# Performance work log

Measured on AMD Instinct MI355X. Metric: run time of the kernel, lower is better.

## Reference

```python
import jax, jax.numpy as jnp
import numpy as np

C = 256
NUM_HEADS = 8
NUM_GROUPS = 32
EPS = 1e-5


def setup_inputs() -> dict:
    key = jax.random.key(0)
    ks = jax.random.split(key, 7)
    B, H, W = 2, 64, 64
    x = jax.random.normal(ks[0], (B, C, H, W), dtype=jnp.float32)
    norm_gamma = jnp.ones((C,), dtype=jnp.float32)
    norm_beta = jnp.zeros((C,), dtype=jnp.float32)
    # 1x1 convs == per-pixel linear layers; store weights as (out_ch, in_ch)
    qkv_w = jax.random.normal(ks[1], (3 * C, C), dtype=jnp.float32) * (1.0 / np.sqrt(C))
    qkv_b = jnp.zeros((3 * C,), dtype=jnp.float32)
    proj_w = jax.random.normal(ks[2], (C, C), dtype=jnp.float32) * (1.0 / np.sqrt(C))
    proj_b = jnp.zeros((C,), dtype=jnp.float32)
    return {"x": x, "norm_gamma": norm_gamma, "norm_beta": norm_beta,
            "qkv_w": qkv_w, "qkv_b": qkv_b, "proj_w": proj_w, "proj_b": proj_b}


def _group_norm(x, gamma, beta):
    B, Cc, H, W = x.shape
    xg = x.reshape(B, NUM_GROUPS, Cc // NUM_GROUPS, H, W)
    mean = xg.mean(axis=(2, 3, 4), keepdims=True)
    var = xg.var(axis=(2, 3, 4), keepdims=True)
    xn = ((xg - mean) * jax.lax.rsqrt(var + EPS)).reshape(B, Cc, H, W)
    return xn * gamma[None, :, None, None] + beta[None, :, None, None]


def reference(x, norm_gamma, norm_beta, qkv_w, qkv_b, proj_w, proj_b):
    B, Cc, H, W = x.shape
    hd = Cc // NUM_HEADS
    N = H * W

    h = _group_norm(x, norm_gamma, norm_beta)
    # 1x1 conv: (3C,C) x (B,C,H,W) -> (B,3C,H,W)
    qkv = jnp.einsum('oc,bchw->bohw', qkv_w, h) + qkv_b[None, :, None, None]
    q, k, v = jnp.split(qkv, 3, axis=1)

    def heads(t):  # (B,C,H,W) -> (B,heads,N,hd)
        return t.reshape(B, NUM_HEADS, hd, N).transpose(0, 1, 3, 2)

    q, k, v = heads(q), heads(k), heads(v)
    scale = hd ** (-0.5)
    attn = jax.nn.softmax(jnp.einsum('bhnd,bhmd->bhnm', q, k) * scale, axis=-1)
    out = jnp.einsum('bhnm,bhmd->bhnd', attn, v)  # (B,heads,N,hd)
    out = out.transpose(0, 1, 3, 2).reshape(B, Cc, H, W)
    out = jnp.einsum('oc,bchw->bohw', proj_w, out) + proj_b[None, :, None, None]
    return x + out
```

## Files before the change

kernel.cpp:

```cpp
#include <hip/hip_runtime.h>
#include <math.h>

#define C_    256
#define NH    8
#define HD_   32
#define NG    32
#define CPG   8
#define NPIX  4096
#define BATCH 2
#define EPSV  1e-5f
#define SLOG2 0.25503489f
#define MF    16.0f
#define KVB   128
#define KSTR  40
#define VSTR  136
#define KPS2  2048

typedef __bf16 bf16x8 __attribute__((ext_vector_type(8)));
typedef __bf16 bf16x4 __attribute__((ext_vector_type(4)));
typedef float  f32x4  __attribute__((ext_vector_type(4)));

__global__ __launch_bounds__(256) void prep_kernel(const float* __restrict__ x,
                                                   float* __restrict__ partial,
                                                   const float* __restrict__ qw,
                                                   const float* __restrict__ pw,
                                                   __bf16* __restrict__ wbq,
                                                   __bf16* __restrict__ wbp) {
    if (blockIdx.x >= 512) {
        const int i = ((blockIdx.x - 512) * 256 + threadIdx.x) * 4;
        const float* src;
        __bf16* dst;
        int off;
        if (i < 768 * 256) { src = qw; dst = wbq; off = i; }
        else { src = pw; dst = wbp; off = i - 768 * 256; }
        const float4 v = *(const float4*)(src + off);
        bf16x4 o;
        o[0] = (__bf16)v.x; o[1] = (__bf16)v.y; o[2] = (__bf16)v.z; o[3] = (__bf16)v.w;
        *(bf16x4*)(dst + off) = o;
        return;
    }
    const int bg = blockIdx.x >> 3;
    const int part = blockIdx.x & 7;
    const int b = bg >> 5, g = bg & 31;
    const float* __restrict__ xp = x + ((size_t)(b * C_ + g * CPG)) * NPIX;

    float s = 0.f, ss = 0.f;
    #pragma unroll
    for (int p = 0; p < 4; ++p) {
        const int i = part * 4096 + p * 1024 + threadIdx.x * 4;
        const float4 v = *(const float4*)(xp + i);
        s  += v.x + v.y + v.z + v.w;
        ss += v.x * v.x + v.y * v.y + v.z * v.z + v.w * v.w;
    }
    #pragma unroll
    for (int off = 32; off; off >>= 1) {
        s  += __shfl_down(s, off);
        ss += __shfl_down(ss, off);
    }
    __shared__ float ls[4], lss[4];
    const int wid = threadIdx.x >> 6, lane = threadIdx.x & 63;
    if (lane == 0) { ls[wid] = s; lss[wid] = ss; }
    __syncthreads();
    if (threadIdx.x == 0) {
        float S = 0.f, SS = 0.f;
        #pragma unroll
        for (int w = 0; w < 4; ++w) { S += ls[w]; SS += lss[w]; }
        partial[bg * 16 + part * 2 + 0] = S;
        partial[bg * 16 + part * 2 + 1] = SS;
    }
}

__global__ __launch_bounds__(256) void qkv_gemm_kernel(const __bf16* __restrict__ wbq,
                                                       const float* __restrict__ bias,
                                                       const float* __restrict__ x,
                                                       const float* __restrict__ partial,
                                                       const float* __restrict__ gamma,
                                                       const float* __restrict__ beta,
                                                       __bf16* __restrict__ Qb,
                                                       __bf16* __restrict__ Kb,
                                                       __bf16* __restrict__ Vb) {
    const int b = blockIdx.z;
    const int n0 = blockIdx.x * 64;
    __shared__ __align__(16) __bf16 tile[64][264];
    __shared__ float gstat[NG][2];

    if (threadIdx.x < NG) {
        float S = 0.f, SS = 0.f;
        #pragma unroll
        for (int p = 0; p < 8; ++p) {
            S  += partial[(b * NG + threadIdx.x) * 16 + p * 2 + 0];
            SS += partial[(b * NG + threadIdx.x) * 16 + p * 2 + 1];
        }
        const float inv_n = 1.0f / (float)(CPG * NPIX);
        const float mean = S * inv_n;
        const float var  = SS * inv_n - mean * mean;
        gstat[threadIdx.x][0] = mean;
        gstat[threadIdx.x][1] = rsqrtf(var + EPSV);
    }
    __syncthreads();

    {
        const int nn = (threadIdx.x & 15) * 4;
        #pragma unroll
        for (int p = 0; p < 16; ++p) {
            const int c = (threadIdx.x >> 4) + p * 16;
            const float4 v = *(const float4*)(x + ((size_t)(b * C_ + c)) * NPIX + n0 + nn);
            const int g = c >> 3;
            const float ga = gamma[c] * gstat[g][1];
            const float be = beta[c] - gstat[g][0] * ga;
            tile[nn + 0][c] = (__bf16)(v.x * ga + be);
            tile[nn + 1][c] = (__bf16)(v.y * ga + be);
            tile[nn + 2][c] = (__bf16)(v.z * ga + be);
            tile[nn + 3][c] = (__bf16)(v.w * ga + be);
        }
    }
    __syncthreads();

    const int wave = threadIdx.x >> 6, lane = threadIdx.x & 63;
    const int col = lane & 15, g = lane >> 4;
    const int m0 = blockIdx.y * 128 + wave * 32;

    f32x4 acc[2][4];
    #pragma unroll
    for (int i = 0; i < 2; ++i)
        #pragma unroll
        for (int j = 0; j < 4; ++j) acc[i][j] = (f32x4){0.f, 0.f, 0.f, 0.f};

    #pragma unroll
    for (int c0 = 0; c0 < C_; c0 += 32) {
        bf16x8 la[2], lb[4];
        #pragma unroll
        for (int mb = 0; mb < 2; ++mb)
            la[mb] = *(const bf16x8*)(wbq + (size_t)(m0 + mb * 16 + col) * C_ + c0 + g * 8);
        #pragma unroll
        for (int nb = 0; nb < 4; ++nb)
            lb[nb] = *(const bf16x8*)(&tile[nb * 16 + col][c0 + g * 8]);
        #pragma unroll
        for (int mb = 0; mb < 2; ++mb)
            #pragma unroll
            for (int nb = 0; nb < 4; ++nb)
                acc[mb][nb] = __builtin_amdgcn_mfma_f32_16x16x32_bf16(la[mb], lb[nb], acc[mb][nb], 0, 0, 0);
    }

    #pragma unroll
    for (int mb = 0; mb < 2; ++mb) {
        const int mbase = m0 + mb * 16 + 4 * g;
        const float4 b4 = *(const float4*)(bias + mbase);
        const int route = mbase >> 8;
        const int bh = b * NH + ((mbase >> 5) & 7);
        const int d0 = mbase & 31;
        #pragma unroll
        for (int nb = 0; nb < 4; ++nb) {
            const int n = n0 + nb * 16 + col;
            f32x4 v = acc[mb][nb];
            v[0] += b4.x; v[1] += b4.y; v[2] += b4.z; v[3] += b4.w;
            if (route == 0) {
                bf16x4 o;
                #pragma unroll
                for (int r = 0; r < 4; ++r) o[r] = (__bf16)(v[r] * SLOG2);
                *(bf16x4*)(Qb + (((size_t)bh * NPIX + n) << 5) + d0) = o;
            } else if (route == 1) {
                bf16x4 o;
                #pragma unroll
                for (int r = 0; r < 4; ++r) o[r] = (__bf16)v[r];
                *(bf16x4*)(Kb + (((size_t)bh * NPIX + n) << 5) + d0) = o;
            } else {
                #pragma unroll
                for (int r = 0; r < 4; ++r)
                    Vb[((size_t)bh * HD_ + d0 + r) * NPIX + n] = (__bf16)v[r];
            }
        }
    }
}

__global__ __launch_bounds__(512) void attn_kernel(const __bf16* __restrict__ Qb,
                                                   const __bf16* __restrict__ Kb,
                                                   const __bf16* __restrict__ Vb,
                                                   __bf16* __restrict__ aot) {
    __shared__ __align__(16) char smem[75776];
    __bf16 (*Ks)[2][KVB][KSTR] = (__bf16 (*)[2][KVB][KSTR])(smem);
    __bf16 (*Vs)[2][HD_][VSTR] = (__bf16 (*)[2][HD_][VSTR])(smem + 40960);
    float* pbuf = (float*)smem;

    const int id = blockIdx.x;
    const int h = id & 7;
    const int rest = id >> 3;
    const int b = rest >> 5;
    const int qt = rest & 31;

    const int wave = threadIdx.x >> 6, lane = threadIdx.x & 63;
    const int hw = wave >> 2, wv = wave & 3;
    const int col = lane & 15, g = lane >> 4;
    const int bh = b * NH + h;
    const int q0 = qt * 128 + wv * 32;

    const __bf16* __restrict__ qp = Qb + ((size_t)bh * NPIX + q0) * HD_;
    const __bf16* __restrict__ kp = Kb + ((size_t)bh * NPIX + hw * KPS2) * HD_;
    const __bf16* __restrict__ vp = Vb + (size_t)bh * HD_ * NPIX + hw * KPS2;

    const int sk_key = wv * 16 + (lane >> 2);
    const int sk_seg = (lane & 3) * 8;
    const int sv_d   = wv * 8 + (lane >> 3);
    const int sv_seg = (lane & 7) * 8;
    const int vslot  = (sv_seg & 32) + ((((sv_seg & 15) >> 2) << 3)) + (((sv_seg >> 4) & 1) << 2);
    const __bf16* __restrict__ kg = kp + (size_t)sk_key * HD_ + sk_seg;
    const __bf16* __restrict__ vg = vp + (size_t)sv_d * NPIX + sv_seg;

    const bf16x8 fq0 = *(const bf16x8*)(qp + col * HD_ + g * 8);
    const bf16x8 fq1 = *(const bf16x8*)(qp + (16 + col) * HD_ + g * 8);

    bf16x8 ones;
    #pragma unroll
    for (int j = 0; j < 8; ++j) ones[j] = (__bf16)1.0f;
    const f32x4 mfc = {-MF, -MF, -MF, -MF};

    f32x4 acc00 = {0.f,0.f,0.f,0.f}, acc01 = {0.f,0.f,0.f,0.f};
    f32x4 acc10 = {0.f,0.f,0.f,0.f}, acc11 = {0.f,0.f,0.f,0.f};
    f32x4 accL0 = {0.f,0.f,0.f,0.f}, accL1 = {0.f,0.f,0.f,0.f};

    {
        const bf16x8 rk0 = *(const bf16x8*)(kg);
        const bf16x8 rk1 = *(const bf16x8*)(kg + (size_t)64 * HD_);
        const bf16x8 rv0 = *(const bf16x8*)(vg);
        const bf16x8 rv1 = *(const bf16x8*)(vg + 64);
        *(bf16x8*)&Ks[hw][0][sk_key][sk_seg]      = rk0;
        *(bf16x8*)&Ks[hw][0][sk_key + 64][sk_seg] = rk1;
        bf16x4 lo, hi;
        #pragma unroll
        for (int j = 0; j < 4; ++j) { lo[j] = rv0[j]; hi[j] = rv0[4 + j]; }
        *(bf16x4*)&Vs[hw][0][sv_d][vslot]     = lo;
        *(bf16x4*)&Vs[hw][0][sv_d][vslot + 8] = hi;
        #pragma unroll
        for (int j = 0; j < 4; ++j) { lo[j] = rv1[j]; hi[j] = rv1[4 + j]; }
        *(bf16x4*)&Vs[hw][0][sv_d][vslot + 64]     = lo;
        *(bf16x4*)&Vs[hw][0][sv_d][vslot + 64 + 8] = hi;
    }
    __syncthreads();

    const int nt = KPS2 / KVB;
    for (int t = 0; t < nt; ++t) {
        const int cur = t & 1;
        bf16x8 nk0, nk1, nv0, nv1;
        const bool more = (t + 1 < nt);
        {
            const size_t koff = (size_t)(more ? (t + 1) * KVB : 0);
            nk0 = *(const bf16x8*)(kg + koff * HD_);
            nk1 = *(const bf16x8*)(kg + (koff + 64) * HD_);
            nv0 = *(const bf16x8*)(vg + koff);
            nv1 = *(const bf16x8*)(vg + koff + 64);
        }

        #pragma unroll
        for (int kk = 0; kk < KVB; kk += 32) {
            const bf16x8 fk0 = *(const bf16x8*)(&Ks[hw][cur][kk + col][g * 8]);
            const bf16x8 fk1 = *(const bf16x8*)(&Ks[hw][cur][kk + 16 + col][g * 8]);
            const bf16x8 fv0 = *(const bf16x8*)(&Vs[hw][cur][col][kk + 8 * g]);
            const bf16x8 fv1 = *(const bf16x8*)(&Vs[hw][cur][col + 16][kk + 8 * g]);

            f32x4 s00 = __builtin_amdgcn_mfma_f32_16x16x32_bf16(fk0, fq0, mfc, 0, 0, 0);
            f32x4 s10 = __builtin_amdgcn_mfma_f32_16x16x32_bf16(fk1, fq0, mfc, 0, 0, 0);
            f32x4 s01 = __builtin_amdgcn_mfma_f32_16x16x32_bf16(fk0, fq1, mfc, 0, 0, 0);
            f32x4 s11 = __builtin_amdgcn_mfma_f32_16x16x32_bf16(fk1, fq1, mfc, 0, 0, 0);

            float p0[8], p1[8];
            #pragma unroll
            for (int r = 0; r < 4; ++r) {
                p0[r]     = __builtin_amdgcn_exp2f(s00[r]);
                p0[4 + r] = __builtin_amdgcn_exp2f(s10[r]);
                p1[r]     = __builtin_amdgcn_exp2f(s01[r]);
                p1[4 + r] = __builtin_amdgcn_exp2f(s11[r]);
            }

            bf16x8 fp0, fp1;
            #pragma unroll
            for (int j = 0; j < 8; ++j) { fp0[j] = (__bf16)p0[j]; fp1[j] = (__bf16)p1[j]; }

            accL0 = __builtin_amdgcn_mfma_f32_16x16x32_bf16(ones, fp0, accL0, 0, 0, 0);
            accL1 = __builtin_amdgcn_mfma_f32_16x16x32_bf16(ones, fp1, accL1, 0, 0, 0);
            acc00 = __builtin_amdgcn_mfma_f32_16x16x32_bf16(fv0, fp0, acc00, 0, 0, 0);
            acc01 = __builtin_amdgcn_mfma_f32_16x16x32_bf16(fv1, fp0, acc01, 0, 0, 0);
            acc10 = __builtin_amdgcn_mfma_f32_16x16x32_bf16(fv0, fp1, acc10, 0, 0, 0);
            acc11 = __builtin_amdgcn_mfma_f32_16x16x32_bf16(fv1, fp1, acc11, 0, 0, 0);
        }

        if (more) {
            *(bf16x8*)&Ks[hw][cur ^ 1][sk_key][sk_seg]      = nk0;
            *(bf16x8*)&Ks[hw][cur ^ 1][sk_key + 64][sk_seg] = nk1;
            bf16x4 lo, hi;
            #pragma unroll
            for (int j = 0; j < 4; ++j) { lo[j] = nv0[j]; hi[j] = nv0[4 + j]; }
            *(bf16x4*)&Vs[hw][cur ^ 1][sv_d][vslot]     = lo;
            *(bf16x4*)&Vs[hw][cur ^ 1][sv_d][vslot + 8] = hi;
            #pragma unroll
            for (int j = 0; j < 4; ++j) { lo[j] = nv1[j]; hi[j] = nv1[4 + j]; }
            *(bf16x4*)&Vs[hw][cur ^ 1][sv_d][vslot + 64]     = lo;
            *(bf16x4*)&Vs[hw][cur ^ 1][sv_d][vslot + 64 + 8] = hi;
        }
        __syncthreads();
    }

    float l0 = accL0[0], l1 = accL1[0];

    if (hw == 1) {
        float* pp = pbuf + ((size_t)wv * 64 + lane) * 20;
        *(f32x4*)(pp + 0)  = acc00;
        *(f32x4*)(pp + 4)  = acc01;
        *(f32x4*)(pp + 8)  = acc10;
        *(f32x4*)(pp + 12) = acc11;
        pp[16] = l0; pp[17] = l1;
    }
    __syncthreads();
    if (hw == 0) {
        const float* pp = pbuf + ((size_t)wv * 64 + lane) * 20;
        const f32x4 b00 = *(const f32x4*)(pp + 0);
        const f32x4 b01 = *(const f32x4*)(pp + 4);
        const f32x4 b10 = *(const f32x4*)(pp + 8);
        const f32x4 b11 = *(const f32x4*)(pp + 12);
        #pragma unroll
        for (int r = 0; r < 4; ++r) {
            acc00[r] += b00[r]; acc01[r] += b01[r];
            acc10[r] += b10[r]; acc11[r] += b11[r];
        }
        const float inv0 = 1.0f / (l0 + pp[16]);
        const float inv1 = 1.0f / (l1 + pp[17]);
        const int cb = h * HD_ + 4 * g;
        {
            __bf16* op = aot + ((size_t)(b * NPIX) + q0 + col) * C_ + cb;
            bf16x4 o0, o1;
            #pragma unroll
            for (int r = 0; r < 4; ++r) { o0[r] = (__bf16)(acc00[r] * inv0); o1[r] = (__bf16)(acc01[r] * inv0); }
            *(bf16x4*)(op) = o0;
            *(bf16x4*)(op + 16) = o1;
        }
        {
            __bf16* op = aot + ((size_t)(b * NPIX) + q0 + 16 + col) * C_ + cb;
            bf16x4 o0, o1;
            #pragma unroll
            for (int r = 0; r < 4; ++r) { o0[r] = (__bf16)(acc10[r] * inv1); o1[r] = (__bf16)(acc11[r] * inv1); }
            *(bf16x4*)(op) = o0;
            *(bf16x4*)(op + 16) = o1;
        }
    }
}

__global__ __launch_bounds__(256) void proj_gemm_kernel(const __bf16* __restrict__ wbp,
                                                        const float* __restrict__ bias,
                                                        const __bf16* __restrict__ aot,
                                                        const float* __restrict__ x,
                                                        float* __restrict__ out) {
    const int b = blockIdx.z;
    const int wave = threadIdx.x >> 6, lane = threadIdx.x & 63;
    const int col = lane & 15, g = lane >> 4;
    const int n0 = blockIdx.x * 64 + (wave & 1) * 32;
    const int m0 = blockIdx.y * 64 + (wave >> 1) * 32;
    const __bf16* __restrict__ ap = aot + (size_t)b * NPIX * C_;

    f32x4 acc[2][2];
    #pragma unroll
    for (int i = 0; i < 2; ++i)
        #pragma unroll
        for (int j = 0; j < 2; ++j) acc[i][j] = (f32x4){0.f, 0.f, 0.f, 0.f};

    #pragma unroll
    for (int c0 = 0; c0 < C_; c0 += 32) {
        bf16x8 la[2], lb[2];
        #pragma unroll
        for (int mb = 0; mb < 2; ++mb)
            la[mb] = *(const bf16x8*)(wbp + (size_t)(m0 + mb * 16 + col) * C_ + c0 + g * 8);
        #pragma unroll
        for (int nb = 0; nb < 2; ++nb)
            lb[nb] = *(const bf16x8*)(ap + (size_t)(n0 + nb * 16 + col) * C_ + c0 + g * 8);
        #pragma unroll
        for (int mb = 0; mb < 2; ++mb)
            #pragma unroll
            for (int nb = 0; nb < 2; ++nb)
                acc[mb][nb] = __builtin_amdgcn_mfma_f32_16x16x32_bf16(la[mb], lb[nb], acc[mb][nb], 0, 0, 0);
    }

    #pragma unroll
    for (int mb = 0; mb < 2; ++mb) {
        const int mbase = m0 + mb * 16 + 4 * g;
        const float4 b4 = *(const float4*)(bias + mbase);
        const float bias_r[4] = {b4.x, b4.y, b4.z, b4.w};
        #pragma unroll
        for (int nb = 0; nb < 2; ++nb) {
            const int n = n0 + nb * 16 + col;
            #pragma unroll
            for (int r = 0; r < 4; ++r) {
                const size_t idx = ((size_t)(b * C_ + mbase + r)) * NPIX + n;
                out[idx] = acc[mb][nb][r] + bias_r[r] + x[idx];
            }
        }
    }
}

extern "C" void kernel_launch(void* const* d_in, const int* in_sizes, int n_in,
                              void* d_out, int out_size, void* d_ws, size_t ws_size,
                              hipStream_t stream) {
    (void)in_sizes; (void)n_in; (void)out_size; (void)ws_size;
    const float* x      = (const float*)d_in[0];
    const float* gamma  = (const float*)d_in[1];
    const float* beta   = (const float*)d_in[2];
    const float* qkv_w  = (const float*)d_in[3];
    const float* qkv_b  = (const float*)d_in[4];
    const float* proj_w = (const float*)d_in[5];
    const float* proj_b = (const float*)d_in[6];
    float* out = (float*)d_out;

    char* ws = (char*)d_ws;
    __bf16* wbq     = (__bf16*)(ws);
    __bf16* wbp     = (__bf16*)(ws + 0x60000);
    float*  partial = (float*) (ws + 0x80000);
    __bf16* Qb      = (__bf16*)(ws + 0x500000);
    __bf16* Kb      = (__bf16*)(ws + 0x900000);
    __bf16* Vb      = (__bf16*)(ws + 0xD00000);
    __bf16* aot     = (__bf16*)(ws + 0x1100000);

    prep_kernel<<<dim3(768), dim3(256), 0, stream>>>(x, partial, qkv_w, proj_w, wbq, wbp);
    qkv_gemm_kernel<<<dim3(NPIX / 64, 768 / 128, BATCH), dim3(256), 0, stream>>>(
        wbq, qkv_b, x, partial, gamma, beta, Qb, Kb, Vb);
    attn_kernel<<<dim3(32 * NH * BATCH), dim3(512), 0, stream>>>(Qb, Kb, Vb, aot);
    proj_gemm_kernel<<<dim3(NPIX / 64, C_ / 64, BATCH), dim3(256), 0, stream>>>(wbp, proj_b, aot, x, out);
}
```

Baseline: 79.10 us.

## Split attention keys four ways with 64 queries per wave

Reorganises the attention block so its 8 waves form four key-split groups of two, instead of two groups of four. Each wave now handles 64 queries instead of 32, with a smaller 64-key tile per step. Every K/V fragment read from shared memory is reused across twice as many queries, cutting LDS traffic per MFMA. The cost is more accumulator registers per wave, a larger shared-memory footprint, and a three-way partial-sum reduction at the end instead of one.

New measurement: 86.67 us. +9.6%, slower.

```diff
diff --git a/kernel.cpp b/kernel.cpp
--- a/kernel.cpp
+++ b/kernel.cpp
@@ -11,10 +11,10 @@
 #define EPSV  1e-5f
 #define SLOG2 0.25503489f
 #define MF    16.0f
-#define KVB   128
+#define KVB   64
 #define KSTR  40
-#define VSTR  136
-#define KPS2  2048
+#define VSTR  72
+#define KPS4  1024
 
 typedef __bf16 bf16x8 __attribute__((ext_vector_type(8)));
 typedef __bf16 bf16x4 __attribute__((ext_vector_type(4)));
@@ -177,7 +177,7 @@
                                                    const __bf16* __restrict__ Kb,
                                                    const __bf16* __restrict__ Vb,
                                                    __bf16* __restrict__ aot) {
-    __shared__ __align__(16) char smem[75776];
+    __shared__ __align__(16) char smem[77824];
     __bf16 (*Ks)[2][KVB][KSTR] = (__bf16 (*)[2][KVB][KSTR])(smem);
     __bf16 (*Vs)[2][HD_][VSTR] = (__bf16 (*)[2][HD_][VSTR])(smem + 40960);
     float* pbuf = (float*)smem;
@@ -189,42 +189,47 @@
     const int qt = rest & 31;
 
     const int wave = threadIdx.x >> 6, lane = threadIdx.x & 63;
-    const int hw = wave >> 2, wv = wave & 3;
+    const int hw = wave >> 1, wv = wave & 1;
     const int col = lane & 15, g = lane >> 4;
     const int bh = b * NH + h;
-    const int q0 = qt * 128 + wv * 32;
+    const int q0 = qt * 128 + wv * 64;
 
     const __bf16* __restrict__ qp = Qb + ((size_t)bh * NPIX + q0) * HD_;
-    const __bf16* __restrict__ kp = Kb + ((size_t)bh * NPIX + hw * KPS2) * HD_;
-    const __bf16* __restrict__ vp = Vb + (size_t)bh * HD_ * NPIX + hw * KPS2;
+    const __bf16* __restrict__ kp = Kb + ((size_t)bh * NPIX + hw * KPS4) * HD_;
+    const __bf16* __restrict__ vp = Vb + (size_t)bh * HD_ * NPIX + hw * KPS4;
 
     const int sk_key = wv * 16 + (lane >> 2);
     const int sk_seg = (lane & 3) * 8;
-    const int sv_d   = wv * 8 + (lane >> 3);
-    const int sv_seg = (lane & 7) * 8;
-    const int vslot  = (sv_seg & 32) + ((((sv_seg & 15) >> 2) << 3)) + (((sv_seg >> 4) & 1) << 2);
+    const int sv_d   = wv * 16 + (lane >> 2);
+    const int sv_seg = (lane & 3) * 8;
+    const int vslot  = (((sv_seg & 15) >> 2) << 3) + (((sv_seg >> 4) & 1) << 2);
     const __bf16* __restrict__ kg = kp + (size_t)sk_key * HD_ + sk_seg;
     const __bf16* __restrict__ vg = vp + (size_t)sv_d * NPIX + sv_seg;
 
-    const bf16x8 fq0 = *(const bf16x8*)(qp + col * HD_ + g * 8);
-    const bf16x8 fq1 = *(const bf16x8*)(qp + (16 + col) * HD_ + g * 8);
+    const bf16x8 fqA = *(const bf16x8*)(qp + col * HD_ + g * 8);
+    const bf16x8 fqB = *(const bf16x8*)(qp + (16 + col) * HD_ + g * 8);
+    const bf16x8 fqC = *(const bf16x8*)(qp + (32 + col) * HD_ + g * 8);
+    const bf16x8 fqD = *(const bf16x8*)(qp + (48 + col) * HD_ + g * 8);
 
     bf16x8 ones;
     #pragma unroll
     for (int j = 0; j < 8; ++j) ones[j] = (__bf16)1.0f;
     const f32x4 mfc = {-MF, -MF, -MF, -MF};
 
-    f32x4 acc00 = {0.f,0.f,0.f,0.f}, acc01 = {0.f,0.f,0.f,0.f};
-    f32x4 acc10 = {0.f,0.f,0.f,0.f}, acc11 = {0.f,0.f,0.f,0.f};
-    f32x4 accL0 = {0.f,0.f,0.f,0.f}, accL1 = {0.f,0.f,0.f,0.f};
+    f32x4 accA0 = {0.f,0.f,0.f,0.f}, accA1 = {0.f,0.f,0.f,0.f};
+    f32x4 accB0 = {0.f,0.f,0.f,0.f}, accB1 = {0.f,0.f,0.f,0.f};
+    f32x4 accC0 = {0.f,0.f,0.f,0.f}, accC1 = {0.f,0.f,0.f,0.f};
+    f32x4 accD0 = {0.f,0.f,0.f,0.f}, accD1 = {0.f,0.f,0.f,0.f};
+    f32x4 accLA = {0.f,0.f,0.f,0.f}, accLB = {0.f,0.f,0.f,0.f};
+    f32x4 accLC = {0.f,0.f,0.f,0.f}, accLD = {0.f,0.f,0.f,0.f};
 
     {
         const bf16x8 rk0 = *(const bf16x8*)(kg);
-        const bf16x8 rk1 = *(const bf16x8*)(kg + (size_t)64 * HD_);
+        const bf16x8 rk1 = *(const bf16x8*)(kg + (size_t)32 * HD_);
         const bf16x8 rv0 = *(const bf16x8*)(vg);
-        const bf16x8 rv1 = *(const bf16x8*)(vg + 64);
+        const bf16x8 rv1 = *(const bf16x8*)(vg + 32);
         *(bf16x8*)&Ks[hw][0][sk_key][sk_seg]      = rk0;
-        *(bf16x8*)&Ks[hw][0][sk_key + 64][sk_seg] = rk1;
+        *(bf16x8*)&Ks[hw][0][sk_key + 32][sk_seg] = rk1;
         bf16x4 lo, hi;
         #pragma unroll
         for (int j = 0; j < 4; ++j) { lo[j] = rv0[j]; hi[j] = rv0[4 + j]; }
@@ -232,12 +237,12 @@
         *(bf16x4*)&Vs[hw][0][sv_d][vslot + 8] = hi;
         #pragma unroll
         for (int j = 0; j < 4; ++j) { lo[j] = rv1[j]; hi[j] = rv1[4 + j]; }
-        *(bf16x4*)&Vs[hw][0][sv_d][vslot + 64]     = lo;
-        *(bf16x4*)&Vs[hw][0][sv_d][vslot + 64 + 8] = hi;
+        *(bf16x4*)&Vs[hw][0][sv_d][vslot + 32]     = lo;
+        *(bf16x4*)&Vs[hw][0][sv_d][vslot + 32 + 8] = hi;
     }
     __syncthreads();
 
-    const int nt = KPS2 / KVB;
+    const int nt = KPS4 / KVB;
     for (int t = 0; t < nt; ++t) {
         const int cur = t & 1;
         bf16x8 nk0, nk1, nv0, nv1;
@@ -245,9 +250,9 @@
         {
             const size_t koff = (size_t)(more ? (t + 1) * KVB : 0);
             nk0 = *(const bf16x8*)(kg + koff * HD_);
-            nk1 = *(const bf16x8*)(kg + (koff + 64) * HD_);
+            nk1 = *(const bf16x8*)(kg + (koff + 32) * HD_);
             nv0 = *(const bf16x8*)(vg + koff);
-            nv1 = *(const bf16x8*)(vg + koff + 64);
+            nv1 = *(const bf16x8*)(vg + koff + 32);
         }
 
         #pragma unroll
@@ -257,35 +262,45 @@
             const bf16x8 fv0 = *(const bf16x8*)(&Vs[hw][cur][col][kk + 8 * g]);
             const bf16x8 fv1 = *(const bf16x8*)(&Vs[hw][cur][col + 16][kk + 8 * g]);
 
-            f32x4 s00 = __builtin_amdgcn_mfma_f32_16x16x32_bf16(fk0, fq0, mfc, 0, 0, 0);
-            f32x4 s10 = __builtin_amdgcn_mfma_f32_16x16x32_bf16(fk1, fq0, mfc, 0, 0, 0);
-            f32x4 s01 = __builtin_amdgcn_mfma_f32_16x16x32_bf16(fk0, fq1, mfc, 0, 0, 0);
-            f32x4 s11 = __builtin_amdgcn_mfma_f32_16x16x32_bf16(fk1, fq1, mfc, 0, 0, 0);
-
-            float p0[8], p1[8];
+            f32x4 sA0 = __builtin_amdgcn_mfma_f32_16x16x32_bf16(fk0, fqA, mfc, 0, 0, 0);
+            f32x4 sA1 = __builtin_amdgcn_mfma_f32_16x16x32_bf16(fk1, fqA, mfc, 0, 0, 0);
+            f32x4 sB0 = __builtin_amdgcn_mfma_f32_16x16x32_bf16(fk0, fqB, mfc, 0, 0, 0);
+            f32x4 sB1 = __builtin_amdgcn_mfma_f32_16x16x32_bf16(fk1, fqB, mfc, 0, 0, 0);
+            f32x4 sC0 = __builtin_amdgcn_mfma_f32_16x16x32_bf16(fk0, fqC, mfc, 0, 0, 0);
+            f32x4 sC1 = __builtin_amdgcn_mfma_f32_16x16x32_bf16(fk1, fqC, mfc, 0, 0, 0);
+            f32x4 sD0 = __builtin_amdgcn_mfma_f32_16x16x32_bf16(fk0, fqD, mfc, 0, 0, 0);
+            f32x4 sD1 = __builtin_amdgcn_mfma_f32_16x16x32_bf16(fk1, fqD, mfc, 0, 0, 0);
+
+            bf16x8 fpA, fpB, fpC, fpD;
             #pragma unroll
             for (int r = 0; r < 4; ++r) {
-                p0[r]     = __builtin_amdgcn_exp2f(s00[r]);
-                p0[4 + r] = __builtin_amdgcn_exp2f(s10[r]);
-                p1[r]     = __builtin_amdgcn_exp2f(s01[r]);
-                p1[4 + r] = __builtin_amdgcn_exp2f(s11[r]);
+                fpA[r]     = (__bf16)__builtin_amdgcn_exp2f(sA0[r]);
+                fpA[4 + r] = (__bf16)__builtin_amdgcn_exp2f(sA1[r]);
+                fpB[r]     = (__bf16)__builtin_amdgcn_exp2f(sB0[r]);
+                fpB[4 + r] = (__bf16)__builtin_amdgcn_exp2f(sB1[r]);
+                fpC[r]     = (__bf16)__builtin_amdgcn_exp2f(sC0[r]);
+                fpC[4 + r] = (__bf16)__builtin_amdgcn_exp2f(sC1[r]);
+                fpD[r]     = (__bf16)__builtin_amdgcn_exp2f(sD0[r]);
+                fpD[4 + r] = (__bf16)__builtin_amdgcn_exp2f(sD1[r]);
             }
 
-            bf16x8 fp0, fp1;
-            #pragma unroll
-            for (int j = 0; j < 8; ++j) { fp0[j] = (__bf16)p0[j]; fp1[j] = (__bf16)p1[j]; }
-
-            accL0 = __builtin_amdgcn_mfma_f32_16x16x32_bf16(ones, fp0, accL0, 0, 0, 0);
-            accL1 = __builtin_amdgcn_mfma_f32_16x16x32_bf16(ones, fp1, accL1, 0, 0, 0);
-            acc00 = __builtin_amdgcn_mfma_f32_16x16x32_bf16(fv0, fp0, acc00, 0, 0, 0);
-            acc01 = __builtin_amdgcn_mfma_f32_16x16x32_bf16(fv1, fp0, acc01, 0, 0, 0);
-            acc10 = __builtin_amdgcn_mfma_f32_16x16x32_bf16(fv0, fp1, acc10, 0, 0, 0);
-            acc11 = __builtin_amdgcn_mfma_f32_16x16x32_bf16(fv1, fp1, acc11, 0, 0, 0);
+            accLA = __builtin_amdgcn_mfma_f32_16x16x32_bf16(ones, fpA, accLA, 0, 0, 0);
+            accLB = __builtin_amdgcn_mfma_f32_16x16x32_bf16(ones, fpB, accLB, 0, 0, 0);
+            accLC = __builtin_amdgcn_mfma_f32_16x16x32_bf16(ones, fpC, accLC, 0, 0, 0);
+            accLD = __builtin_amdgcn_mfma_f32_16x16x32_bf16(ones, fpD, accLD, 0, 0, 0);
+            accA0 = __builtin_amdgcn_mfma_f32_16x16x32_bf16(fv0, fpA, accA0, 0, 0, 0);
+            accA1 = __builtin_amdgcn_mfma_f32_16x16x32_bf16(fv1, fpA, accA1, 0, 0, 0);
+            accB0 = __builtin_amdgcn_mfma_f32_16x16x32_bf16(fv0, fpB, accB0, 0, 0, 0);
+            accB1 = __builtin_amdgcn_mfma_f32_16x16x32_bf16(fv1, fpB, accB1, 0, 0, 0);
+            accC0 = __builtin_amdgcn_mfma_f32_16x16x32_bf16(fv0, fpC, accC0, 0, 0, 0);
+            accC1 = __builtin_amdgcn_mfma_f32_16x16x32_bf16(fv1, fpC, accC1, 0, 0, 0);
+            accD0 = __builtin_amdgcn_mfma_f32_16x16x32_bf16(fv0, fpD, accD0, 0, 0, 0);
+            accD1 = __builtin_amdgcn_mfma_f32_16x16x32_bf16(fv1, fpD, accD1, 0, 0, 0);
         }
 
         if (more) {
             *(bf16x8*)&Ks[hw][cur ^ 1][sk_key][sk_seg]      = nk0;
-            *(bf16x8*)&Ks[hw][cur ^ 1][sk_key + 64][sk_seg] = nk1;
+            *(bf16x8*)&Ks[hw][cur ^ 1][sk_key + 32][sk_seg] = nk1;
             bf16x4 lo, hi;
             #pragma unroll
             for (int j = 0; j < 4; ++j) { lo[j] = nv0[j]; hi[j] = nv0[4 + j]; }
@@ -293,50 +308,50 @@
             *(bf16x4*)&Vs[hw][cur ^ 1][sv_d][vslot + 8] = hi;
             #pragma unroll
             for (int j = 0; j < 4; ++j) { lo[j] = nv1[j]; hi[j] = nv1[4 + j]; }
-            *(bf16x4*)&Vs[hw][cur ^ 1][sv_d][vslot + 64]     = lo;
-            *(bf16x4*)&Vs[hw][cur ^ 1][sv_d][vslot + 64 + 8] = hi;
+            *(bf16x4*)&Vs[hw][cur ^ 1][sv_d][vslot + 32]     = lo;
+            *(bf16x4*)&Vs[hw][cur ^ 1][sv_d][vslot + 32 + 8] = hi;
         }
         __syncthreads();
     }
 
-    float l0 = accL0[0], l1 = accL1[0];
-
-    if (hw == 1) {
-        float* pp = pbuf + ((size_t)wv * 64 + lane) * 20;
-        *(f32x4*)(pp + 0)  = acc00;
-        *(f32x4*)(pp + 4)  = acc01;
-        *(f32x4*)(pp + 8)  = acc10;
-        *(f32x4*)(pp + 12) = acc11;
-        pp[16] = l0; pp[17] = l1;
+    if (hw != 0) {
+        float* pp = pbuf + ((size_t)((hw - 1) * 128 + wv * 64 + lane)) * 36;
+        *(f32x4*)(pp + 0)  = accA0; *(f32x4*)(pp + 4)  = accA1;
+        *(f32x4*)(pp + 8)  = accB0; *(f32x4*)(pp + 12) = accB1;
+        *(f32x4*)(pp + 16) = accC0; *(f32x4*)(pp + 20) = accC1;
+        *(f32x4*)(pp + 24) = accD0; *(f32x4*)(pp + 28) = accD1;
+        pp[32] = accLA[0]; pp[33] = accLB[0]; pp[34] = accLC[0]; pp[35] = accLD[0];
     }
     __syncthreads();
     if (hw == 0) {
-        const float* pp = pbuf + ((size_t)wv * 64 + lane) * 20;
-        const f32x4 b00 = *(const f32x4*)(pp + 0);
-        const f32x4 b01 = *(const f32x4*)(pp + 4);
-        const f32x4 b10 = *(const f32x4*)(pp + 8);
-        const f32x4 b11 = *(const f32x4*)(pp + 12);
-        #pragma unroll
-        for (int r = 0; r < 4; ++r) {
-            acc00[r] += b00[r]; acc01[r] += b01[r];
-            acc10[r] += b10[r]; acc11[r] += b11[r];
-        }
-        const float inv0 = 1.0f / (l0 + pp[16]);
-        const float inv1 = 1.0f / (l1 + pp[17]);
+        float lA = accLA[0], lB = accLB[0], lC = accLC[0], lD = accLD[0];
+        #pragma unroll
+        for (int s = 0; s < 3; ++s) {
+            const float* pp = pbuf + ((size_t)(s * 128 + wv * 64 + lane)) * 36;
+            const f32x4 a0 = *(const f32x4*)(pp + 0),  a1 = *(const f32x4*)(pp + 4);
+            const f32x4 b0 = *(const f32x4*)(pp + 8),  b1 = *(const f32x4*)(pp + 12);
+            const f32x4 c0 = *(const f32x4*)(pp + 16), c1 = *(const f32x4*)(pp + 20);
+            const f32x4 d0 = *(const f32x4*)(pp + 24), d1 = *(const f32x4*)(pp + 28);
+            #pragma unroll
+            for (int r = 0; r < 4; ++r) {
+                accA0[r] += a0[r]; accA1[r] += a1[r];
+                accB0[r] += b0[r]; accB1[r] += b1[r];
+                accC0[r] += c0[r]; accC1[r] += c1[r];
+                accD0[r] += d0[r]; accD1[r] += d1[r];
+            }
+            lA += pp[32]; lB += pp[33]; lC += pp[34]; lD += pp[35];
+        }
+        const float iA = 1.0f / lA, iB = 1.0f / lB, iC = 1.0f / lC, iD = 1.0f / lD;
         const int cb = h * HD_ + 4 * g;
-        {
-            __bf16* op = aot + ((size_t)(b * NPIX) + q0 + col) * C_ + cb;
+        #pragma unroll
+        for (int qf = 0; qf < 4; ++qf) {
+            const f32x4* a0 = (qf == 0) ? &accA0 : (qf == 1) ? &accB0 : (qf == 2) ? &accC0 : &accD0;
+            const f32x4* a1 = (qf == 0) ? &accA1 : (qf == 1) ? &accB1 : (qf == 2) ? &accC1 : &accD1;
+            const float inv = (qf == 0) ? iA : (qf == 1) ? iB : (qf == 2) ? iC : iD;
+            __bf16* op = aot + ((size_t)(b * NPIX) + q0 + qf * 16 + col) * C_ + cb;
             bf16x4 o0, o1;
             #pragma unroll
-            for (int r = 0; r < 4; ++r) { o0[r] = (__bf16)(acc00[r] * inv0); o1[r] = (__bf16)(acc01[r] * inv0); }
-            *(bf16x4*)(op) = o0;
-            *(bf16x4*)(op + 16) = o1;
-        }
-        {
-            __bf16* op = aot + ((size_t)(b * NPIX) + q0 + 16 + col) * C_ + cb;
-            bf16x4 o0, o1;
-            #pragma unroll
-            for (int r = 0; r < 4; ++r) { o0[r] = (__bf16)(acc10[r] * inv1); o1[r] = (__bf16)(acc11[r] * inv1); }
+            for (int r = 0; r < 4; ++r) { o0[r] = (__bf16)((*a0)[r] * inv); o1[r] = (__bf16)((*a1)[r] * inv); }
             *(bf16x4*)(op) = o0;
             *(bf16x4*)(op + 16) = o1;
         }
```
